# Kernel tuning notes

Hardware: AMD Instinct MI355X
Metric: run time of the kernel (lower is better)

Reference implementation:

```python
import jax, jax.numpy as jnp
import numpy as np

# --- SLAYER SRM-alpha parameters (ncaltech101 yaml) ---
THETA = 10.0      # spike threshold
TAU_SR = 10.0     # synaptic response time constant
TAU_REF = 1.0     # refractory time constant
SCALE_REF = 2.0   # refractory scale
TAU_RHO = 1.0     # surrogate-pdf time constant
SCALE_RHO = 1.0   # surrogate-pdf scale
TS = 1.0          # simulation step
T_SAMPLE = 300    # number of time steps


def _alpha_kernel(tau, mult, Ts=TS, t_sample=T_SAMPLE):
    # SLAYER _calculateAlphaKernel: eps(t) = mult * t/tau * exp(1 - t/tau), truncated
    eps = []
    for t in np.arange(0.0, t_sample, Ts):
        v = mult * t / tau * np.exp(1.0 - t / tau)
        if abs(v) < 0.01 and t > tau:
            break
        eps.append(v)
    return np.asarray(eps, np.float32)

SRM_KERNEL = _alpha_kernel(TAU_SR, 1.0)                 # psp kernel, length ~76
REF_KERNEL = _alpha_kernel(TAU_REF, -SCALE_REF * THETA)  # refractory kernel, length ~12


def psp(x):
    """Causal temporal filter with the SRM alpha kernel. x: (B, N, T)."""
    eps = jnp.asarray(SRM_KERNEL)
    K = eps.shape[0]
    B, N, T = x.shape
    lhs = x.reshape(B * N, 1, T)
    rhs = eps[::-1].reshape(1, 1, K)  # flip: conv_general_dilated is correlation
    y = jax.lax.conv_general_dilated(lhs, rhs, window_strides=(1,),
                                     padding=[(K - 1, 0)],
                                     dimension_numbers=("NCH", "OIH", "NCH"))
    return y.reshape(B, N, T)


def _spike_scan(u):
    """Threshold + refractory reset over time. u: (B, N, T) -> (spikes, u_eff)."""
    ref = jnp.asarray(REF_KERNEL)  # (K,)
    B, N, T = u.shape
    K = ref.shape[0]

    def step(buf, u_t):
        # buf[..., 0] is the accumulated refractory contribution for this step
        u_eff = u_t + buf[..., 0]
        s = (u_eff >= THETA).astype(u_t.dtype)
        buf = buf + s[..., None] * ref            # add refractory kernel from new spikes
        buf = jnp.concatenate([buf[:, :, 1:], jnp.zeros_like(buf[:, :, :1])], axis=-1)
        return buf, (s, u_eff)

    buf0 = jnp.zeros((B, N, K), u.dtype)
    _, (s, u_eff) = jax.lax.scan(step, buf0, jnp.moveaxis(u, -1, 0))
    return jnp.moveaxis(s, 0, -1), jnp.moveaxis(u_eff, 0, -1)


@jax.custom_vjp
def spike(u):
    return _spike_scan(u)[0]


def _spike_fwd(u):
    s, u_eff = _spike_scan(u)
    return s, u_eff


def _spike_bwd(u_eff, g):
    # SLAYER surrogate gradient: scaleRho/(tauRho*theta) * exp(-|u - theta|/(tauRho*theta))
    tau = TAU_RHO * THETA
    pdf = (SCALE_RHO / tau) * jnp.exp(-jnp.abs(u_eff - THETA) / tau)
    return (g * pdf,)


spike.defvjp(_spike_fwd, _spike_bwd)


def setup_inputs() -> dict:
    key = jax.random.key(0)
    k1, k2, k3 = jax.random.split(key, 3)
    B, C, H, W, T = 2, 2, 200, 156, T_SAMPLE
    inp = (jax.random.uniform(k1, (B, C, H, W, T)) < 0.05).astype(jnp.float32)
    w1 = jax.random.normal(k2, (800, C * H * W), dtype=jnp.float32) * 0.05
    w2 = jax.random.normal(k3, (100, 800), dtype=jnp.float32) * 0.05
    return {"input": inp, "w1": w1, "w2": w2}


def reference(input, w1, w2):
    B, T = input.shape[0], input.shape[-1]
    x = input.reshape(B, -1, T)                      # (B, 62400, T)
    x = spike(psp(jnp.einsum("bft,of->bot", x, w1)))  # (B, 800, T)
    x = spike(psp(jnp.einsum("bft,of->bot", x, w2)))  # (B, 100, T)
    return x
```

## Files before the change

kernel.cpp:

```cpp
#include <hip/hip_runtime.h>

#define F1 62400
#define O1 800
#define O2N 100
#define TT 300
#define BB 2
#define NWRD 975
#define KSRM 77
#define KREF 11
#define M32 25
#define NPAD 640
#define NDIG 4
#define KSPL 10
#define WPS 98
#define BSTRIDE ((size_t)NPAD * 4)

#define NB_K1 2438

typedef unsigned long long u64;
typedef int i32x4 __attribute__((ext_vector_type(4)));

#define CSWZ(c) ((c) ^ ((((c) >> 4) & 3) << 1))

#define OFF_CONST 0ull
#define OFF_Z1P  1024ull
#define OFF_S1T  (OFF_Z1P + 40960000ull)
#define OFF_XBW  (OFF_S1T + 1920000ull)
#define OFF_Z1F  (OFF_XBW + 4992000ull)
#define OFF_U1   (OFF_Z1F + 3840000ull)
#define OFF_U2   (OFF_U1 + 3840000ull)
#define NEED_SPARSE (OFF_U2 + 480000ull)

__global__ void k0_init(double* c) {
    int k = threadIdx.x;
    if (k < KSRM) {
        double v = ((double)k / 10.0) * exp(1.0 - (double)k / 10.0);
        c[k] = (double)(float)v;
    }
    if (k < KREF) {
        double v = -20.0 * (double)k * exp(1.0 - (double)k);
        c[80 + k] = (double)(float)v;
    }
}

__global__ __launch_bounds__(256) void k_pre(const float* __restrict__ x,
                                             u64* __restrict__ xbw,
                                             double* __restrict__ cst) {
    int blk = blockIdx.x;
    if (blk < NB_K1) {
        const int NTG = 5;
        int gw = (blk * 256 + (int)threadIdx.x) >> 6;
        int lane = threadIdx.x & 63;
        if (gw >= BB * NWRD * NTG) return;
        int b  = gw / (NWRD * NTG);
        int r  = gw % (NWRD * NTG);
        int fw = r / NTG;
        int tg = r % NTG;
        int t = tg * 64 + lane;
        bool act = (t < TT);
        int tc = act ? t : 0;
        const float* xp = x + ((size_t)(b * F1 + (fw << 6))) * TT + tc;
        unsigned lo = 0, hi = 0;
        #pragma unroll
        for (int j = 0; j < 32; ++j)
            lo |= (xp[(size_t)j * TT] > 0.5f ? 1u : 0u) << j;
        #pragma unroll
        for (int j = 0; j < 32; ++j)
            hi |= (xp[(size_t)(j + 32) * TT] > 0.5f ? 1u : 0u) << j;
        u64 mval = act ? (((u64)hi << 32) | lo) : 0ull;
        xbw[(size_t)fw * NPAD + b * 320 + t] = mval;
    } else {
        int k = threadIdx.x;
        if (k < KSRM) {
            double v = ((double)k / 10.0) * exp(1.0 - (double)k / 10.0);
            cst[k] = (double)(float)v;
        }
        if (k < KREF) {
            double v = -20.0 * (double)k * exp(1.0 - (double)k);
            cst[80 + k] = (double)(float)v;
        }
    }
}

__device__ __forceinline__ void quant4(float4 f, unsigned dw[4]) {
    float ff[4] = {f.x, f.y, f.z, f.w};
    dw[0] = 0; dw[1] = 0; dw[2] = 0; dw[3] = 0;
    #pragma unroll
    for (int e = 0; e < 4; ++e) {
        int v  = (int)rintf(ff[e] * 2147483648.0f);
        int r0 = (v + 128) >> 8;
        int r1 = (r0 + 128) >> 8;
        int r2 = (r1 + 128) >> 8;
        dw[0] |= (unsigned)(v  & 0xFF) << (8 * e);
        dw[1] |= (unsigned)(r0 & 0xFF) << (8 * e);
        dw[2] |= (unsigned)(r1 & 0xFF) << (8 * e);
        dw[3] |= (unsigned)(r2 & 0xFF) << (8 * e);
    }
}

#define K3_TILE(BV, TTI)                                                           \
    {                                                                              \
        i32x4 bf;                                                                  \
        _Pragma("unroll")                                                          \
        for (int i_ = 0; i_ < 4; ++i_)                                             \
            bf[i_] = (int)((((BV >> (4 * i_)) & 0xFu) * 0x00204081u) & 0x01010101u); \
        _Pragma("unroll")                                                          \
        for (int h_ = 0; h_ < 2; ++h_)                                             \
            _Pragma("unroll")                                                      \
            for (int d_ = 0; d_ < NDIG; ++d_)                                      \
                acc[TTI][h_][d_] = __builtin_amdgcn_mfma_i32_16x16x64_i8(          \
                    a[h_][d_], bf, acc[TTI][h_][d_], 0, 0, 0);                     \
    }

#define K_ITER(S, FQ, FI, BU0, BU1, BU2, BU3, BU4, BL0, BL1, BL2, BL3, BL4)        \
    {                                                                              \
        int s_ = (S);                                                              \
        if (s_ < steps) {                                                          \
            int pf = s_ + 2; if (pf > steps - 1) pf = steps - 1;                   \
            FI = *(const float4*)(fbase + (size_t)pf * 64);                        \
            int sn = s_ + 1; if (sn > steps - 1) sn = steps - 1;                   \
            const unsigned short* bpn = bp0 + (size_t)sn * BSTRIDE;                \
            BL0 = bpn[0]; BL1 = bpn[64]; BL2 = bpn[128]; BL3 = bpn[192]; BL4 = bpn[256]; \
            const char* lp = &Abuf[s_ & 1][0];                                     \
            i32x4 a[2][4];                                                         \
            _Pragma("unroll")                                                      \
            for (int h_ = 0; h_ < 2; ++h_)                                         \
                _Pragma("unroll")                                                  \
                for (int d_ = 0; d_ < NDIG; ++d_)                                  \
                    a[h_][d_] = *(const i32x4*)(lp + h_ * 4096 + d_ * 1024 + lofs); \
            K3_TILE(BU0, 0)                                                        \
            K3_TILE(BU1, 1)                                                        \
            K3_TILE(BU2, 2)                                                        \
            K3_TILE(BU3, 3)                                                        \
            K3_TILE(BU4, 4)                                                        \
            unsigned dwq[4];                                                       \
            quant4(FQ, dwq);                                                       \
            char* wb = &Abuf[(s_ + 1) & 1][0] + wofs;                              \
            *(unsigned*)(wb)        = dwq[0];                                      \
            *(unsigned*)(wb + 1024) = dwq[1];                                      \
            *(unsigned*)(wb + 2048) = dwq[2];                                      \
            *(unsigned*)(wb + 3072) = dwq[3];                                      \
        }                                                                          \
        __syncthreads();                                                           \
    }

__global__ __launch_bounds__(512, 2) void k3m2(const float* __restrict__ w1,
                                               const u64* __restrict__ xbw,
                                               u64* __restrict__ z1p) {
    __shared__ __align__(16) char Abuf[2][8192];
    int m32 = blockIdx.x, ksl = blockIdx.y;
    int tid = threadIdx.x;
    int l = tid & 63, wid = tid >> 6;
    int o  = tid >> 4;
    int kq = tid & 15;

    int wl0 = ksl * WPS;
    int wend = wl0 + WPS; if (wend > NWRD) wend = NWRD;
    int steps = wend - wl0;

    i32x4 acc[5][2][NDIG];
    #pragma unroll
    for (int i = 0; i < 5; ++i)
        #pragma unroll
        for (int h = 0; h < 2; ++h)
            #pragma unroll
            for (int d = 0; d < NDIG; ++d) acc[i][h][d] = (i32x4){0, 0, 0, 0};

    const float* fbase = w1 + (size_t)(m32 * 32 + o) * F1 + (size_t)wl0 * 64 + kq * 4;
    const unsigned short* bp0 =
        (const unsigned short*)((const char*)xbw
            + ((size_t)wl0 * NPAD
               + (size_t)(wid * 80 + (l & 15))) * 8
            + (l >> 4) * 2);
    const int lofs = CSWZ(l) * 16;
    const int wc = (kq >> 2) * 16 + (o & 15);
    const int wofs = (o >> 4) * 4096 + CSWZ(wc) * 16 + (kq & 3) * 4;

    float4 fA, fB, fC;
    unsigned bA0, bA1, bA2, bA3, bA4;
    unsigned bB0, bB1, bB2, bB3, bB4;
    unsigned bC0, bC1, bC2, bC3, bC4;

    fA = *(const float4*)(fbase);
    {
        unsigned dwq[4];
        quant4(fA, dwq);
        char* wb = &Abuf[0][0] + wofs;
        *(unsigned*)(wb)        = dwq[0];
        *(unsigned*)(wb + 1024) = dwq[1];
        *(unsigned*)(wb + 2048) = dwq[2];
        *(unsigned*)(wb + 3072) = dwq[3];
    }
    fB = *(const float4*)(fbase + ((steps > 1) ? 64 : 0));
    bA0 = bp0[0]; bA1 = bp0[64]; bA2 = bp0[128]; bA3 = bp0[192]; bA4 = bp0[256];
    __syncthreads();

    int smax3 = ((steps + 2) / 3) * 3;
    #pragma unroll 1
    for (int sb = 0; sb < smax3; sb += 3) {
        K_ITER(sb,     fB, fC, bA0, bA1, bA2, bA3, bA4, bB0, bB1, bB2, bB3, bB4)
        K_ITER(sb + 1, fC, fA, bB0, bB1, bB2, bB3, bB4, bC0, bC1, bC2, bC3, bC4)
        K_ITER(sb + 2, fA, fB, bC0, bC1, bC2, bC3, bC4, bA0, bA1, bA2, bA3, bA4)
    }

    u64* zp = z1p + (size_t)ksl * O1 * NPAD;
    #pragma unroll
    for (int tt = 0; tt < 5; ++tt) {
        int n = wid * 80 + tt * 16 + (l & 15);
        #pragma unroll
        for (int h = 0; h < 2; ++h) {
            #pragma unroll
            for (int r = 0; r < 4; ++r) {
                int oo = m32 * 32 + h * 16 + (l >> 4) * 4 + r;
                long long c = (long long)acc[tt][h][0][r]
                            + ((long long)acc[tt][h][1][r] << 8)
                            + ((long long)acc[tt][h][2][r] << 16)
                            + ((long long)acc[tt][h][3][r] << 24);
                zp[(size_t)oo * NPAD + n] = (u64)c;
            }
        }
    }
}

__global__ __launch_bounds__(256) void k_dense_gemm1(const float* __restrict__ x,
                                                     const float* __restrict__ w1,
                                                     double* __restrict__ z1) {
    int lin = blockIdx.x;
    int ot = lin % 25; int tt = (lin / 25) % 5; int b = lin / 125;
    int t0 = tt * 64, o0 = ot * 32;
    __shared__ float xs[64][64];
    __shared__ float wsh[32][64];
    int ti = threadIdx.x & 63, og = threadIdx.x >> 6;
    double dacc[8] = {0, 0, 0, 0, 0, 0, 0, 0};
    for (int fc = 0; fc < F1; fc += 64) {
        __syncthreads();
        for (int e = threadIdx.x; e < 64 * 64; e += 256) {
            int r = e >> 6, c = e & 63;
            int t = t0 + c;
            xs[r][c] = (t < TT) ? x[((size_t)b * F1 + fc + r) * TT + t] : 0.0f;
        }
        for (int e = threadIdx.x; e < 32 * 64; e += 256) {
            int r = e >> 6, c = e & 63;
            wsh[r][c] = w1[(size_t)(o0 + r) * F1 + fc + c];
        }
        __syncthreads();
        float facc[8] = {0, 0, 0, 0, 0, 0, 0, 0};
        for (int ff = 0; ff < 64; ++ff) {
            float xv = xs[ff][ti];
            #pragma unroll
            for (int oo = 0; oo < 8; ++oo) facc[oo] += wsh[og * 8 + oo][ff] * xv;
        }
        #pragma unroll
        for (int oo = 0; oo < 8; ++oo) dacc[oo] += (double)facc[oo];
    }
    int t = t0 + ti;
    if (t < TT) {
        #pragma unroll
        for (int oo = 0; oo < 8; ++oo) {
            int o = o0 + og * 8 + oo;
            z1[((size_t)(b * O1 + o)) * TT + t] = dacc[oo];
        }
    }
}

__global__ __launch_bounds__(320) void k_conv1(const u64* __restrict__ z1p,
                                               const double* __restrict__ z1f,
                                               double* __restrict__ u1,
                                               const double* __restrict__ cst,
                                               int mode) {
    __shared__ double zs[TT];
    __shared__ double ck[KSRM];
    int row = blockIdx.x;
    int b = row / O1, o = row % O1;
    int t = threadIdx.x;
    if (t < KSRM) ck[t] = cst[t];
    if (t < TT) {
        double z;
        if (mode == 0) {
            long long c = 0;
            size_t base = (size_t)o * NPAD + b * 320 + t;
            #pragma unroll
            for (int g = 0; g < KSPL; ++g)
                c += (long long)z1p[(size_t)g * O1 * NPAD + base];
            z = (double)c * 4.656612873077393e-10;
        } else {
            z = z1f[(size_t)row * TT + t];
        }
        zs[t] = z;
    }
    __syncthreads();
    if (t < TT) {
        int kmax = t < (KSRM - 1) ? t : (KSRM - 1);
        double acc = 0.0;
        for (int k = 0; k <= kmax; ++k) acc += ck[k] * zs[t - k];
        u1[(size_t)row * TT + t] = acc;
    }
}

__global__ __launch_bounds__(64) void k_scan(const double* __restrict__ u,
                                             float* __restrict__ s,
                                             const double* __restrict__ cst,
                                             int nrows) {
    int row = blockIdx.x * 64 + threadIdx.x;
    if (row >= nrows) return;
    double rk1 = cst[81], rk2 = cst[82], rk3 = cst[83], rk4 = cst[84];
    double rk5 = cst[85], rk6 = cst[86], rk7 = cst[87], rk8 = cst[88];
    double rk9 = cst[89], rk10 = cst[90];
    const double* ur = u + (size_t)row * TT;
    float* sr = s + (size_t)row * TT;
    double buf[30];
    #pragma unroll
    for (int j = 0; j < 30; ++j) buf[j] = ur[j];
    unsigned h = 0;
    #pragma unroll 1
    for (int tb = 0; tb < TT; tb += 30) {
        double nxt[30];
        #pragma unroll
        for (int j = 0; j < 30; ++j) {
            int tn = tb + 30 + j; if (tn > TT - 1) tn = TT - 1;
            nxt[j] = ur[tn];
        }
        #pragma unroll
        for (int j = 0; j < 30; ++j) {
            double a  = ((h & 1u)   ? rk1 : 0.0) + ((h & 2u)   ? rk2  : 0.0);
            double b2 = ((h & 4u)   ? rk3 : 0.0) + ((h & 8u)   ? rk4  : 0.0);
            double c2 = ((h & 16u)  ? rk5 : 0.0) + ((h & 32u)  ? rk6  : 0.0);
            double d2 = ((h & 64u)  ? rk7 : 0.0) + ((h & 128u) ? rk8  : 0.0);
            double e2 = ((h & 256u) ? rk9 : 0.0) + ((h & 512u) ? rk10 : 0.0);
            double ueff = buf[j] + (((a + b2) + (c2 + d2)) + e2);
            unsigned sp = (ueff >= 10.0) ? 1u : 0u;
            sr[tb + j] = (float)sp;
            h = (h << 1) | sp;
        }
        #pragma unroll
        for (int j = 0; j < 30; ++j) buf[j] = nxt[j];
    }
}

__global__ __launch_bounds__(320) void k_gemm2c(const float* __restrict__ s1t,
                                                const float* __restrict__ w2,
                                                double* __restrict__ u2,
                                                const double* __restrict__ cst) {
    __shared__ float wsm[O1];
    __shared__ double zs[TT];
    __shared__ double ck[KSRM];
    int bo = blockIdx.x;
    int b = bo / O2N, o2 = bo % O2N;
    int t = threadIdx.x;
    if (t < KSRM) ck[t] = cst[t];
    for (int f = t; f < O1; f += 320) wsm[f] = w2[(size_t)o2 * O1 + f];
    __syncthreads();
    if (t < TT) {
        double acc = 0.0;
        #pragma unroll 4
        for (int f = 0; f < O1; ++f)
            acc += (double)(wsm[f] * s1t[((size_t)(b * O1 + f)) * TT + t]);
        zs[t] = acc;
    }
    __syncthreads();
    if (t < TT) {
        int kmax = t < (KSRM - 1) ? t : (KSRM - 1);
        double acc = 0.0;
        for (int k = 0; k <= kmax; ++k) acc += ck[k] * zs[t - k];
        u2[(size_t)bo * TT + t] = acc;
    }
}

extern "C" void kernel_launch(void* const* d_in, const int* in_sizes, int n_in,
                              void* d_out, int out_size, void* d_ws, size_t ws_size,
                              hipStream_t stream) {
    const float* x  = (const float*)d_in[0];
    const float* w1 = (const float*)d_in[1];
    const float* w2 = (const float*)d_in[2];
    float* out = (float*)d_out;
    char* ws = (char*)d_ws;

    double* cst = (double*)(ws + OFF_CONST);
    u64*    z1p = (u64*)   (ws + OFF_Z1P);
    float*  s1t = (float*) (ws + OFF_S1T);
    u64*    xbw = (u64*)   (ws + OFF_XBW);
    double* z1f = (double*)(ws + OFF_Z1F);
    double* u1  = (double*)(ws + OFF_U1);
    double* u2  = (double*)(ws + OFF_U2);

    int mode;
    if (ws_size >= NEED_SPARSE) {
        mode = 0;
        k_pre<<<NB_K1 + 1, 256, 0, stream>>>(x, xbw, cst);
        k3m2<<<dim3(M32, KSPL), 512, 0, stream>>>(w1, xbw, z1p);
    } else {
        mode = 1;
        k0_init<<<1, 128, 0, stream>>>(cst);
        k_dense_gemm1<<<250, 256, 0, stream>>>(x, w1, z1f);
    }

    k_conv1<<<BB * O1, 320, 0, stream>>>(z1p, z1f, u1, cst, mode);
    k_scan<<<(BB * O1 + 63) / 64, 64, 0, stream>>>(u1, s1t, cst, BB * O1);
    k_gemm2c<<<BB * O2N, 320, 0, stream>>>(s1t, w2, u2, cst);
    k_scan<<<(BB * O2N + 63) / 64, 64, 0, stream>>>(u2, out, cst, BB * O2N);
    (void)in_sizes; (void)n_in; (void)out_size;
}
```

Baseline: 270.3 us.

## Transpose layer-1 spike output and double K-split of sparse GEMM

The first spike scan now writes its output time-major (per batch, t rows of 800 features), so the second GEMM can read each thread's feature vector contiguously with float4 loads. The sparse first GEMM's split-K factor is doubled (KSPL 20, WPS 49), with workspace offsets enlarged for the bigger partial-sum buffer. The trade-offs are strided stores in the scan and more partials to reduce in conv1, in exchange for more parallelism in the big GEMM.

```diff
diff --git a/kernel.cpp b/kernel.cpp
--- a/kernel.cpp
+++ b/kernel.cpp
@@ -11,8 +11,8 @@
 #define M32 25
 #define NPAD 640
 #define NDIG 4
-#define KSPL 10
-#define WPS 98
+#define KSPL 20
+#define WPS 49
 #define BSTRIDE ((size_t)NPAD * 4)
 
 #define NB_K1 2438
@@ -24,8 +24,8 @@
 
 #define OFF_CONST 0ull
 #define OFF_Z1P  1024ull
-#define OFF_S1T  (OFF_Z1P + 40960000ull)
-#define OFF_XBW  (OFF_S1T + 1920000ull)
+#define OFF_S1T  (OFF_Z1P + 81920000ull)
+#define OFF_XBW  (OFF_S1T + 2048000ull)
 #define OFF_Z1F  (OFF_XBW + 4992000ull)
 #define OFF_U1   (OFF_Z1F + 3840000ull)
 #define OFF_U2   (OFF_U1 + 3840000ull)
@@ -300,14 +300,24 @@
 __global__ __launch_bounds__(64) void k_scan(const double* __restrict__ u,
                                              float* __restrict__ s,
                                              const double* __restrict__ cst,
-                                             int nrows) {
+                                             int nrows, int tmode) {
     int row = blockIdx.x * 64 + threadIdx.x;
     if (row >= nrows) return;
     double rk1 = cst[81], rk2 = cst[82], rk3 = cst[83], rk4 = cst[84];
     double rk5 = cst[85], rk6 = cst[86], rk7 = cst[87], rk8 = cst[88];
     double rk9 = cst[89], rk10 = cst[90];
     const double* ur = u + (size_t)row * TT;
-    float* sr = s + (size_t)row * TT;
+    float* sbase;
+    size_t sstep;
+    if (tmode) {
+        int b = (row >= O1) ? 1 : 0;
+        int f = row - b * O1;
+        sbase = s + (size_t)(b * 320) * O1 + f;
+        sstep = O1;
+    } else {
+        sbase = s + (size_t)row * TT;
+        sstep = 1;
+    }
     double buf[30];
     #pragma unroll
     for (int j = 0; j < 30; ++j) buf[j] = ur[j];
@@ -329,7 +339,7 @@
             double e2 = ((h & 256u) ? rk9 : 0.0) + ((h & 512u) ? rk10 : 0.0);
             double ueff = buf[j] + (((a + b2) + (c2 + d2)) + e2);
             unsigned sp = (ueff >= 10.0) ? 1u : 0u;
-            sr[tb + j] = (float)sp;
+            sbase[(size_t)(tb + j) * sstep] = (float)sp;
             h = (h << 1) | sp;
         }
         #pragma unroll
@@ -351,10 +361,16 @@
     for (int f = t; f < O1; f += 320) wsm[f] = w2[(size_t)o2 * O1 + f];
     __syncthreads();
     if (t < TT) {
+        const float4* sp = (const float4*)(s1t + (size_t)(b * 320 + t) * O1);
         double acc = 0.0;
         #pragma unroll 4
-        for (int f = 0; f < O1; ++f)
-            acc += (double)(wsm[f] * s1t[((size_t)(b * O1 + f)) * TT + t]);
+        for (int ff = 0; ff < O1 / 4; ++ff) {
+            float4 v = sp[ff];
+            acc += (double)(wsm[4 * ff]     * v.x);
+            acc += (double)(wsm[4 * ff + 1] * v.y);
+            acc += (double)(wsm[4 * ff + 2] * v.z);
+            acc += (double)(wsm[4 * ff + 3] * v.w);
+        }
         zs[t] = acc;
     }
     __syncthreads();
@@ -395,8 +411,8 @@
     }
 
     k_conv1<<<BB * O1, 320, 0, stream>>>(z1p, z1f, u1, cst, mode);
-    k_scan<<<(BB * O1 + 63) / 64, 64, 0, stream>>>(u1, s1t, cst, BB * O1);
+    k_scan<<<(BB * O1 + 63) / 64, 64, 0, stream>>>(u1, s1t, cst, BB * O1, 1);
     k_gemm2c<<<BB * O2N, 320, 0, stream>>>(s1t, w2, u2, cst);
-    k_scan<<<(BB * O2N + 63) / 64, 64, 0, stream>>>(u2, out, cst, BB * O2N);
+    k_scan<<<(BB * O2N + 63) / 64, 64, 0, stream>>>(u2, out, cst, BB * O2N, 0);
     (void)in_sizes; (void)n_in; (void)out_size;
 }
```

After: 257.8 us, median of 2. 4.6% less time.
